# Optimization experiments

Hardware: AMD Instinct MI355X
Metric: run time of the kernel (lower is better)

Reference implementation:

```python
import jax, jax.numpy as jnp
import numpy as np

PAD = 16      # ReplicationPad2d(16)
KW = 33       # per-block kernel is 33x33
PATCH = 36    # 36x36 input patch per 4x4 output block
BLK = 4       # output block size


def setup_inputs() -> dict:
    key = jax.random.key(0)
    k1, k2 = jax.random.split(key)
    inputImg = jax.random.normal(k1, (1, 3, 512, 512), dtype=jnp.float32)
    Kernels = jax.random.uniform(k2, (1, KW * KW, 512 // BLK, 512 // BLK), dtype=jnp.float32)
    return {"inputImg": inputImg, "Kernels": Kernels}


def reference(inputImg, Kernels):
    B, C, H, W = inputImg.shape
    HB, WB = H // BLK, W // BLK
    # replication pad == edge pad
    padded = jnp.pad(inputImg, ((0, 0), (0, 0), (PAD, PAD), (PAD, PAD)), mode="edge")
    # gather overlapping 36x36 patches, one per 4x4 block (stride 4)
    idx_h = BLK * jnp.arange(HB)[:, None] + jnp.arange(PATCH)[None, :]  # [HB,36]
    idx_w = BLK * jnp.arange(WB)[:, None] + jnp.arange(PATCH)[None, :]  # [WB,36]
    tmp = padded[:, :, idx_h, :]            # [B,C,HB,36,Wp]
    patches = tmp[:, :, :, :, idx_w]        # [B,C,HB,36,WB,36]
    # per-block 33x33 kernel: Kernels[0, u*33+v, h, w] -> K[u,v,h,w]
    K = Kernels[0].reshape(KW, KW, HB, WB)
    # valid conv: out offset (oi,oj) in the 4x4 block
    rows = []
    for oi in range(BLK):
        cols = []
        for oj in range(BLK):
            win = patches[:, :, :, oi:oi + KW, :, oj:oj + KW]  # [B,C,HB,33,WB,33]
            cols.append(jnp.einsum("bchuwv,uvhw->bchw", win, K))
        rows.append(jnp.stack(cols, axis=-1))   # [B,C,HB,WB,4]
    out = jnp.stack(rows, axis=-2)              # [B,C,HB,WB,4,4]
    out = out.transpose(0, 1, 2, 4, 3, 5).reshape(B, C, H, W)
    return out
```

## Files before the change

### kernel.cpp

```cpp
#include <hip/hip_runtime.h>

#define HH 512
#define WW 512
#define PD 544
#define PADN (3 * PD * PD)
#define OUTN (3 * HH * WW)
#define NB 128
#define KSTR 16384

__global__ __launch_bounds__(256) void pad_kernel(const float* __restrict__ img,
                                                  unsigned short* __restrict__ gpad,
                                                  float* __restrict__ out) {
    int idx = blockIdx.x * 256 + threadIdx.x;
    if (idx < OUTN) out[idx] = 0.0f;
    if (idx >= PADN) return;
    int c  = idx / (PD * PD);
    int r  = idx - c * (PD * PD);
    int py = r / PD;
    int px = r - py * PD;
    int iy = min(max(py - 16, 0), HH - 1);
    int ix = min(max(px - 16, 0), WW - 1);
    union { float f; unsigned u; } v;
    v.f = img[(c * HH + iy) * WW + ix];
    unsigned u = v.u + 0x7FFFu + ((v.u >> 16) & 1u);
    gpad[idx] = (unsigned short)(u >> 16);
}

__device__ __forceinline__ void async4(const float* g, float* l) {
    __builtin_amdgcn_global_load_lds((const __attribute__((address_space(1))) void*)g,
                                     (__attribute__((address_space(3))) void*)l, 4, 0, 0);
}
__device__ __forceinline__ void async16u(const unsigned short* g, unsigned short* l) {
    __builtin_amdgcn_global_load_lds((const __attribute__((address_space(1))) void*)g,
                                     (__attribute__((address_space(3))) void*)l, 16, 0, 0);
}

__device__ __forceinline__ float bflo(unsigned d) {
    union { unsigned u; float f; } x; x.u = d << 16; return x.f;
}
__device__ __forceinline__ float bfhi(unsigned d) {
    union { unsigned u; float f; } x; x.u = d & 0xFFFF0000u; return x.f;
}

__global__ __launch_bounds__(64) void reblur_kernel(const unsigned short* __restrict__ gpad,
                                                    const float* __restrict__ Kern,
                                                    float* __restrict__ out) {
    __shared__ float s_w[4][33][64];
    __shared__ unsigned short s_img[2][3][296];

    const int lane = threadIdx.x;
    const int s    = blockIdx.x >> 8;
    const int bb   = blockIdx.x & 255;
    const int h    = bb >> 1;
    const int wt   = bb & 1;
    const int p0   = 12 * s;
    const int p1   = p0 + 12;
    const int kofs = h * NB + wt * 64 + lane;

    for (int u = max(0, p0 - 3); u <= p0; ++u)
        for (int v = 0; v < 33; ++v)
            async4(Kern + ((u * 33 + v) * KSTR + kofs), &s_w[u & 3][v][0]);
    if (lane < 36)
        for (int c = 0; c < 3; ++c)
            async16u(gpad + ((size_t)(c * PD + 4 * h + p0) * PD + 256 * wt) + 8 * lane,
                     &s_img[p0 & 1][c][0]);

    float acc[3][4][4];
#pragma unroll
    for (int c = 0; c < 3; ++c)
#pragma unroll
        for (int dy = 0; dy < 4; ++dy)
#pragma unroll
            for (int oj = 0; oj < 4; ++oj) acc[c][dy][oj] = 0.0f;

#pragma unroll 1
    for (int pp = p0; pp < p1; ++pp) {
        asm volatile("s_waitcnt vmcnt(0)" ::: "memory");

        float wreg[33];
        const int u3 = pp - 3;
        if (u3 >= 0) {
#pragma unroll
            for (int v = 0; v < 33; ++v) wreg[v] = s_w[u3 & 3][v][lane];
        }
        asm volatile("s_waitcnt lgkmcnt(0)" ::: "memory");

        if (pp + 1 < p1) {
            const int un = pp + 1;
            if (un <= 32)
                for (int v = 0; v < 33; ++v)
                    async4(Kern + ((un * 33 + v) * KSTR + kofs), &s_w[un & 3][v][0]);
            if (lane < 36)
                for (int c = 0; c < 3; ++c)
                    async16u(gpad + ((size_t)(c * PD + 4 * h + un) * PD + 256 * wt) + 8 * lane,
                             &s_img[un & 1][c][0]);
        }

        float wf[3][36];
        const int slot = pp & 1;
#pragma unroll
        for (int c = 0; c < 3; ++c) {
#pragma unroll
            for (int j = 0; j < 9; ++j) {
                const uint2 d = *(const uint2*)&s_img[slot][c][4 * lane + 4 * j];
                wf[c][4 * j + 0] = bflo(d.x);
                wf[c][4 * j + 1] = bfhi(d.x);
                wf[c][4 * j + 2] = bflo(d.y);
                wf[c][4 * j + 3] = bfhi(d.y);
            }
        }

#pragma unroll
        for (int dy = 0; dy < 3; ++dy) {
            const int u = pp - dy;
            if (u >= 0 && u <= 32) {
                const float* wp = &s_w[u & 3][0][lane];
#pragma unroll
                for (int v = 0; v < 33; ++v) {
                    const float w = wp[v * 64];
#pragma unroll
                    for (int c = 0; c < 3; ++c)
#pragma unroll
                        for (int oj = 0; oj < 4; ++oj)
                            acc[c][dy][oj] = fmaf(wf[c][v + oj], w, acc[c][dy][oj]);
                }
            }
        }
        if (u3 >= 0) {
#pragma unroll
            for (int v = 0; v < 33; ++v) {
#pragma unroll
                for (int c = 0; c < 3; ++c)
#pragma unroll
                    for (int oj = 0; oj < 4; ++oj)
                        acc[c][3][oj] = fmaf(wf[c][v + oj], wreg[v], acc[c][3][oj]);
            }
        }
    }

#pragma unroll
    for (int c = 0; c < 3; ++c)
#pragma unroll
        for (int dy = 0; dy < 4; ++dy) {
            float* op = out + (size_t)(c * HH + 4 * h + dy) * WW + 4 * (wt * 64 + lane);
#pragma unroll
            for (int oj = 0; oj < 4; ++oj) atomicAdd(op + oj, acc[c][dy][oj]);
        }
}

__global__ __launch_bounds__(256) void reblur_naive(const float* __restrict__ img,
                                                    const float* __restrict__ Kern,
                                                    float* __restrict__ out) {
    const int lane = threadIdx.x & 63;
    const int dy   = threadIdx.x >> 6;
    const int c    = blockIdx.x >> 8;
    const int bb   = blockIdx.x & 255;
    const int h    = bb >> 1;
    const int wt   = bb & 1;
    const int wb   = wt * 64 + lane;
    const int y    = 4 * h + dy;

    float acc[4] = {0.f, 0.f, 0.f, 0.f};
    const float* kb = Kern + h * NB + wb;
#pragma unroll 1
    for (int u = 0; u < 33; ++u) {
        const int iy = min(max(y + u - 16, 0), HH - 1);
        float row[36];
#pragma unroll
        for (int e = 0; e < 36; ++e) {
            const int ix = min(max(4 * wb + e - 16, 0), WW - 1);
            row[e]       = img[(c * HH + iy) * WW + ix];
        }
#pragma unroll
        for (int v = 0; v < 33; ++v) {
            const float w = kb[(u * 33 + v) * KSTR];
#pragma unroll
            for (int oj = 0; oj < 4; ++oj)
                acc[oj] = fmaf(row[v + oj], w, acc[oj]);
        }
    }
    float4 o;
    o.x = acc[0]; o.y = acc[1]; o.z = acc[2]; o.w = acc[3];
    *reinterpret_cast<float4*>(out + (size_t)(c * HH + y) * WW + 4 * wb) = o;
}

extern "C" void kernel_launch(void* const* d_in, const int* in_sizes, int n_in,
                              void* d_out, int out_size, void* d_ws, size_t ws_size,
                              hipStream_t stream) {
    const float* img  = (const float*)d_in[0];
    const float* Kern = (const float*)d_in[1];
    float* out        = (float*)d_out;

    if (ws_size >= (size_t)PADN * sizeof(unsigned short)) {
        unsigned short* gpad = (unsigned short*)d_ws;
        pad_kernel<<<(PADN + 255) / 256, 256, 0, stream>>>(img, gpad, out);
        reblur_kernel<<<768, 64, 0, stream>>>(gpad, Kern, out);
    } else {
        reblur_naive<<<768, 256, 0, stream>>>(img, Kern, out);
    }
}
```

Baseline: 160.1 us.

## Split output rows across two waves per block and partition kernel rows into four chunks

The reblur kernel now uses 128-thread blocks in which each wave owns two of the four output rows of a block. Kernel-row loading is split between the waves: one streams weights into LDS while the other streams image rows into a 4-deep ring. The u-range is split into four chunks (9/8/8/8) over 1024 blocks, replacing three 12-row chunks over 768 blocks. Weights are double-buffered in registers so each loaded row serves two output rows. This cuts per-thread accumulator and register pressure and raises parallelism, at the cost of a block-wide barrier every step and more atomic adds to the output.

```diff
diff --git a/kernel.cpp b/kernel.cpp
--- a/kernel.cpp
+++ b/kernel.cpp
@@ -34,118 +34,124 @@
     __builtin_amdgcn_global_load_lds((const __attribute__((address_space(1))) void*)g,
                                      (__attribute__((address_space(3))) void*)l, 16, 0, 0);
 }
-
-__device__ __forceinline__ float bflo(unsigned d) {
-    union { unsigned u; float f; } x; x.u = d << 16; return x.f;
-}
-__device__ __forceinline__ float bfhi(unsigned d) {
-    union { unsigned u; float f; } x; x.u = d & 0xFFFF0000u; return x.f;
-}
-
-__global__ __launch_bounds__(64) void reblur_kernel(const unsigned short* __restrict__ gpad,
-                                                    const float* __restrict__ Kern,
-                                                    float* __restrict__ out) {
-    __shared__ float s_w[4][33][64];
-    __shared__ unsigned short s_img[2][3][296];
-
-    const int lane = threadIdx.x;
-    const int s    = blockIdx.x >> 8;
-    const int bb   = blockIdx.x & 255;
-    const int h    = bb >> 1;
-    const int wt   = bb & 1;
-    const int p0   = 12 * s;
-    const int p1   = p0 + 12;
-    const int kofs = h * NB + wt * 64 + lane;
-
-    for (int u = max(0, p0 - 3); u <= p0; ++u)
+__device__ __forceinline__ float bflo(unsigned d) { union { unsigned u; float f; } x; x.u = d << 16;         return x.f; }
+__device__ __forceinline__ float bfhi(unsigned d) { union { unsigned u; float f; } x; x.u = d & 0xFFFF0000u; return x.f; }
+
+__global__ __launch_bounds__(128, 3) void reblur_kernel(const unsigned short* __restrict__ gpad,
+                                                        const float* __restrict__ Kern,
+                                                        float* __restrict__ out) {
+    __shared__ float s_w[2][33][64];
+    __shared__ unsigned short s_img[4][3][296];
+
+    const int lane   = threadIdx.x & 63;
+    const int pairId = threadIdx.x >> 6;
+    const int d0     = 2 * pairId;
+    const int uq     = blockIdx.x >> 8;
+    const int bb     = blockIdx.x & 255;
+    const int h      = bb >> 1;
+    const int wt     = bb & 1;
+    const int ua     = (uq == 0) ? 0 : (1 + 8 * uq);
+    const int n      = (uq == 0) ? 9 : 8;
+    const int kofs   = h * NB + wt * 64 + lane;
+    const int rbase  = 4 * h + ua;
+
+    if (pairId == 0) {
+#pragma unroll
         for (int v = 0; v < 33; ++v)
-            async4(Kern + ((u * 33 + v) * KSTR + kofs), &s_w[u & 3][v][0]);
-    if (lane < 36)
-        for (int c = 0; c < 3; ++c)
-            async16u(gpad + ((size_t)(c * PD + 4 * h + p0) * PD + 256 * wt) + 8 * lane,
-                     &s_img[p0 & 1][c][0]);
-
-    float acc[3][4][4];
+            async4(Kern + ((ua * 33 + v) * KSTR + kofs), &s_w[0][v][0]);
+    } else if (lane < 36) {
+#pragma unroll
+        for (int rr = 0; rr < 3; ++rr)
+#pragma unroll
+            for (int c = 0; c < 3; ++c)
+                async16u(gpad + ((size_t)(c * PD + rbase + rr) * PD + 256 * wt) + 8 * lane,
+                         &s_img[(rbase + rr) & 3][c][0]);
+    }
+
+    float wA[33], wB[33];
+    float accE[3][4], accO[3][4];
 #pragma unroll
     for (int c = 0; c < 3; ++c)
 #pragma unroll
-        for (int dy = 0; dy < 4; ++dy)
-#pragma unroll
-            for (int oj = 0; oj < 4; ++oj) acc[c][dy][oj] = 0.0f;
+        for (int oj = 0; oj < 4; ++oj) { accE[c][oj] = 0.f; accO[c][oj] = 0.f; }
+
+    auto body = [&](int t, int par, float (&wnew)[33], float (&wold)[33]) {
+        asm volatile("s_waitcnt vmcnt(0)" ::: "memory");
+        __builtin_amdgcn_s_barrier();
+        asm volatile("" ::: "memory");
+
+        const bool doE = (t < n);
+        const bool doO = (t > 0);
+
+        if (doE) {
+            if (pairId == 0) {
+                const int un = ua + t + 1;
+                if (t + 1 < n) {
+#pragma unroll
+                    for (int v = 0; v < 33; ++v)
+                        async4(Kern + ((un * 33 + v) * KSTR + kofs), &s_w[par ^ 1][v][0]);
+                }
+            } else if (lane < 36) {
+                const int r = rbase + t + 3;
+#pragma unroll
+                for (int c = 0; c < 3; ++c)
+                    async16u(gpad + ((size_t)(c * PD + r) * PD + 256 * wt) + 8 * lane,
+                             &s_img[r & 3][c][0]);
+            }
+        }
+
+        if (doE) {
+#pragma unroll
+            for (int v = 0; v < 33; ++v) wnew[v] = s_w[par][v][lane];
+        }
+
+        const int slot = (rbase + d0 + t) & 3;
+#pragma unroll
+        for (int c = 0; c < 3; ++c) {
+            float wf[36];
+            const unsigned short* sp = &s_img[slot][c][4 * lane];
+#pragma unroll
+            for (int j = 0; j < 9; ++j) {
+                const uint2 dd = *(const uint2*)(sp + 4 * j);
+                wf[4 * j + 0] = bflo(dd.x);
+                wf[4 * j + 1] = bfhi(dd.x);
+                wf[4 * j + 2] = bflo(dd.y);
+                wf[4 * j + 3] = bfhi(dd.y);
+            }
+            if (doE) {
+#pragma unroll
+                for (int v = 0; v < 33; ++v)
+#pragma unroll
+                    for (int oj = 0; oj < 4; ++oj)
+                        accE[c][oj] = fmaf(wf[v + oj], wnew[v], accE[c][oj]);
+            }
+            if (doO) {
+#pragma unroll
+                for (int v = 0; v < 33; ++v)
+#pragma unroll
+                    for (int oj = 0; oj < 4; ++oj)
+                        accO[c][oj] = fmaf(wf[v + oj], wold[v], accO[c][oj]);
+            }
+        }
+    };
 
 #pragma unroll 1
-    for (int pp = p0; pp < p1; ++pp) {
-        asm volatile("s_waitcnt vmcnt(0)" ::: "memory");
-
-        float wreg[33];
-        const int u3 = pp - 3;
-        if (u3 >= 0) {
-#pragma unroll
-            for (int v = 0; v < 33; ++v) wreg[v] = s_w[u3 & 3][v][lane];
-        }
-        asm volatile("s_waitcnt lgkmcnt(0)" ::: "memory");
-
-        if (pp + 1 < p1) {
-            const int un = pp + 1;
-            if (un <= 32)
-                for (int v = 0; v < 33; ++v)
-                    async4(Kern + ((un * 33 + v) * KSTR + kofs), &s_w[un & 3][v][0]);
-            if (lane < 36)
-                for (int c = 0; c < 3; ++c)
-                    async16u(gpad + ((size_t)(c * PD + 4 * h + un) * PD + 256 * wt) + 8 * lane,
-                             &s_img[un & 1][c][0]);
-        }
-
-        float wf[3][36];
-        const int slot = pp & 1;
-#pragma unroll
-        for (int c = 0; c < 3; ++c) {
-#pragma unroll
-            for (int j = 0; j < 9; ++j) {
-                const uint2 d = *(const uint2*)&s_img[slot][c][4 * lane + 4 * j];
-                wf[c][4 * j + 0] = bflo(d.x);
-                wf[c][4 * j + 1] = bfhi(d.x);
-                wf[c][4 * j + 2] = bflo(d.y);
-                wf[c][4 * j + 3] = bfhi(d.y);
-            }
-        }
-
-#pragma unroll
-        for (int dy = 0; dy < 3; ++dy) {
-            const int u = pp - dy;
-            if (u >= 0 && u <= 32) {
-                const float* wp = &s_w[u & 3][0][lane];
-#pragma unroll
-                for (int v = 0; v < 33; ++v) {
-                    const float w = wp[v * 64];
-#pragma unroll
-                    for (int c = 0; c < 3; ++c)
-#pragma unroll
-                        for (int oj = 0; oj < 4; ++oj)
-                            acc[c][dy][oj] = fmaf(wf[c][v + oj], w, acc[c][dy][oj]);
-                }
-            }
-        }
-        if (u3 >= 0) {
-#pragma unroll
-            for (int v = 0; v < 33; ++v) {
-#pragma unroll
-                for (int c = 0; c < 3; ++c)
-#pragma unroll
-                    for (int oj = 0; oj < 4; ++oj)
-                        acc[c][3][oj] = fmaf(wf[c][v + oj], wreg[v], acc[c][3][oj]);
-            }
-        }
-    }
-
-#pragma unroll
-    for (int c = 0; c < 3; ++c)
-#pragma unroll
-        for (int dy = 0; dy < 4; ++dy) {
-            float* op = out + (size_t)(c * HH + 4 * h + dy) * WW + 4 * (wt * 64 + lane);
-#pragma unroll
-            for (int oj = 0; oj < 4; ++oj) atomicAdd(op + oj, acc[c][dy][oj]);
-        }
+    for (int t2 = 0; t2 <= n; t2 += 2) {
+        body(t2, 0, wA, wB);
+        if (t2 + 1 <= n) body(t2 + 1, 1, wB, wA);
+    }
+
+    const int xb = 4 * (wt * 64 + lane);
+#pragma unroll
+    for (int c = 0; c < 3; ++c) {
+        float* opE = out + (size_t)(c * HH + 4 * h + d0) * WW + xb;
+        float* opO = opE + WW;
+#pragma unroll
+        for (int oj = 0; oj < 4; ++oj) {
+            atomicAdd(opE + oj, accE[c][oj]);
+            atomicAdd(opO + oj, accO[c][oj]);
+        }
+    }
 }
 
 __global__ __launch_bounds__(256) void reblur_naive(const float* __restrict__ img,
@@ -194,7 +200,7 @@
     if (ws_size >= (size_t)PADN * sizeof(unsigned short)) {
         unsigned short* gpad = (unsigned short*)d_ws;
         pad_kernel<<<(PADN + 255) / 256, 256, 0, stream>>>(img, gpad, out);
-        reblur_kernel<<<768, 64, 0, stream>>>(gpad, Kern, out);
+        reblur_kernel<<<1024, 128, 0, stream>>>(gpad, Kern, out);
     } else {
         reblur_naive<<<768, 256, 0, stream>>>(img, Kern, out);
     }
```

After: 301.5 us. 1.88x slower.

## Restructure reblur into 4-wave blocks splitting kernel rows, weights in registers

Applied to the files above, without the earlier changes.

The reblur kernel now uses 256-thread blocks where each wave handles one output row offset dy, and the 33 kernel rows are split into two halves (17/16) across blocks instead of three 12-row passes. Kernel weights are loaded straight into double-buffered registers instead of staged through LDS, and image rows go into an 8-slot LDS ring shared by the four waves with block barriers. The aim is to cut LDS weight traffic and redundant weight reads, raise occupancy and halve the atomic partial sums. The cost is block-level synchronisation each step and direct global weight loads whose latency must hide behind compute.

```diff
diff --git a/kernel.cpp b/kernel.cpp
--- a/kernel.cpp
+++ b/kernel.cpp
@@ -26,126 +26,104 @@
     gpad[idx] = (unsigned short)(u >> 16);
 }
 
-__device__ __forceinline__ void async4(const float* g, float* l) {
-    __builtin_amdgcn_global_load_lds((const __attribute__((address_space(1))) void*)g,
-                                     (__attribute__((address_space(3))) void*)l, 4, 0, 0);
-}
 __device__ __forceinline__ void async16u(const unsigned short* g, unsigned short* l) {
     __builtin_amdgcn_global_load_lds((const __attribute__((address_space(1))) void*)g,
                                      (__attribute__((address_space(3))) void*)l, 16, 0, 0);
 }
+__device__ __forceinline__ float bflo(unsigned d) { union { unsigned u; float f; } x; x.u = d << 16;         return x.f; }
+__device__ __forceinline__ float bfhi(unsigned d) { union { unsigned u; float f; } x; x.u = d & 0xFFFF0000u; return x.f; }
 
-__device__ __forceinline__ float bflo(unsigned d) {
-    union { unsigned u; float f; } x; x.u = d << 16; return x.f;
-}
-__device__ __forceinline__ float bfhi(unsigned d) {
-    union { unsigned u; float f; } x; x.u = d & 0xFFFF0000u; return x.f;
-}
+__global__ __launch_bounds__(256, 2) void reblur_kernel(const unsigned short* __restrict__ gpad,
+                                                        const float* __restrict__ Kern,
+                                                        float* __restrict__ out) {
+    __shared__ unsigned short s_img[8][3][288];
 
-__global__ __launch_bounds__(64) void reblur_kernel(const unsigned short* __restrict__ gpad,
-                                                    const float* __restrict__ Kern,
-                                                    float* __restrict__ out) {
-    __shared__ float s_w[4][33][64];
-    __shared__ unsigned short s_img[2][3][296];
-
-    const int lane = threadIdx.x;
-    const int s    = blockIdx.x >> 8;
+    const int lane = threadIdx.x & 63;
+    const int dy   = threadIdx.x >> 6;
+    const int uq   = blockIdx.x >> 8;
     const int bb   = blockIdx.x & 255;
     const int h    = bb >> 1;
     const int wt   = bb & 1;
-    const int p0   = 12 * s;
-    const int p1   = p0 + 12;
+    const int ua   = 17 * uq;
+    const int n    = 17 - uq;
     const int kofs = h * NB + wt * 64 + lane;
 
-    for (int u = max(0, p0 - 3); u <= p0; ++u)
-        for (int v = 0; v < 33; ++v)
-            async4(Kern + ((u * 33 + v) * KSTR + kofs), &s_w[u & 3][v][0]);
-    if (lane < 36)
+    if (lane < 36) {
+        const int r = 4 * h + ua + dy;
+#pragma unroll
         for (int c = 0; c < 3; ++c)
-            async16u(gpad + ((size_t)(c * PD + 4 * h + p0) * PD + 256 * wt) + 8 * lane,
-                     &s_img[p0 & 1][c][0]);
+            async16u(gpad + ((size_t)(c * PD + r) * PD + 256 * wt) + 8 * lane,
+                     &s_img[r & 7][c][0]);
+    }
+    float wA[33], wB[33];
+#pragma unroll
+    for (int v = 0; v < 33; ++v)
+        wA[v] = Kern[(size_t)(ua * 33 + v) * KSTR + kofs];
 
-    float acc[3][4][4];
+    float acc[3][4];
 #pragma unroll
     for (int c = 0; c < 3; ++c)
 #pragma unroll
-        for (int dy = 0; dy < 4; ++dy)
-#pragma unroll
-            for (int oj = 0; oj < 4; ++oj) acc[c][dy][oj] = 0.0f;
+        for (int oj = 0; oj < 4; ++oj) acc[c][oj] = 0.0f;
 
-#pragma unroll 1
-    for (int pp = p0; pp < p1; ++pp) {
-        asm volatile("s_waitcnt vmcnt(0)" ::: "memory");
-
-        float wreg[33];
-        const int u3 = pp - 3;
-        if (u3 >= 0) {
-#pragma unroll
-            for (int v = 0; v < 33; ++v) wreg[v] = s_w[u3 & 3][v][lane];
-        }
-        asm volatile("s_waitcnt lgkmcnt(0)" ::: "memory");
-
-        if (pp + 1 < p1) {
-            const int un = pp + 1;
-            if (un <= 32)
-                for (int v = 0; v < 33; ++v)
-                    async4(Kern + ((un * 33 + v) * KSTR + kofs), &s_w[un & 3][v][0]);
-            if (lane < 36)
-                for (int c = 0; c < 3; ++c)
-                    async16u(gpad + ((size_t)(c * PD + 4 * h + un) * PD + 256 * wt) + 8 * lane,
-                             &s_img[un & 1][c][0]);
-        }
-
-        float wf[3][36];
-        const int slot = pp & 1;
-#pragma unroll
-        for (int c = 0; c < 3; ++c) {
-#pragma unroll
-            for (int j = 0; j < 9; ++j) {
-                const uint2 d = *(const uint2*)&s_img[slot][c][4 * lane + 4 * j];
-                wf[c][4 * j + 0] = bflo(d.x);
-                wf[c][4 * j + 1] = bfhi(d.x);
-                wf[c][4 * j + 2] = bflo(d.y);
-                wf[c][4 * j + 3] = bfhi(d.y);
-            }
-        }
-
-#pragma unroll
-        for (int dy = 0; dy < 3; ++dy) {
-            const int u = pp - dy;
-            if (u >= 0 && u <= 32) {
-                const float* wp = &s_w[u & 3][0][lane];
-#pragma unroll
-                for (int v = 0; v < 33; ++v) {
-                    const float w = wp[v * 64];
-#pragma unroll
-                    for (int c = 0; c < 3; ++c)
-#pragma unroll
-                        for (int oj = 0; oj < 4; ++oj)
-                            acc[c][dy][oj] = fmaf(wf[c][v + oj], w, acc[c][dy][oj]);
-                }
-            }
-        }
-        if (u3 >= 0) {
-#pragma unroll
-            for (int v = 0; v < 33; ++v) {
-#pragma unroll
-                for (int c = 0; c < 3; ++c)
-#pragma unroll
-                    for (int oj = 0; oj < 4; ++oj)
-                        acc[c][3][oj] = fmaf(wf[c][v + oj], wreg[v], acc[c][3][oj]);
-            }
-        }
+#define R6_ITER(WCUR, WNXT, TT)                                                  \
+    {                                                                            \
+        const int tt = (TT);                                                     \
+        asm volatile("s_waitcnt vmcnt(0)" ::: "memory");                         \
+        __builtin_amdgcn_s_barrier();                                            \
+        if (tt + 1 < n) {                                                        \
+            const int un = ua + tt + 1;                                          \
+            _Pragma("unroll")                                                    \
+            for (int v = 0; v < 33; ++v)                                         \
+                WNXT[v] = Kern[(size_t)(un * 33 + v) * KSTR + kofs];             \
+            if (dy == (tt & 3) && lane < 36) {                                   \
+                const int r = 4 * h + ua + tt + 4;                               \
+                _Pragma("unroll")                                                \
+                for (int c = 0; c < 3; ++c)                                      \
+                    async16u(gpad + ((size_t)(c * PD + r) * PD + 256 * wt) + 8 * lane, \
+                             &s_img[r & 7][c][0]);                               \
+            }                                                                    \
+        }                                                                        \
+        const int slot = (4 * h + ua + tt + dy) & 7;                             \
+        _Pragma("unroll")                                                        \
+        for (int c = 0; c < 3; ++c) {                                            \
+            float wf[36];                                                        \
+            const unsigned short* sp = &s_img[slot][c][4 * lane];                \
+            _Pragma("unroll")                                                    \
+            for (int j = 0; j < 9; ++j) {                                        \
+                const uint2 dd = *(const uint2*)(sp + 4 * j);                    \
+                wf[4 * j + 0] = bflo(dd.x);                                      \
+                wf[4 * j + 1] = bfhi(dd.x);                                      \
+                wf[4 * j + 2] = bflo(dd.y);                                      \
+                wf[4 * j + 3] = bfhi(dd.y);                                      \
+            }                                                                    \
+            _Pragma("unroll")                                                    \
+            for (int v = 0; v < 33; ++v) {                                       \
+                _Pragma("unroll")                                                \
+                for (int oj = 0; oj < 4; ++oj)                                   \
+                    acc[c][oj] = fmaf(wf[v + oj], WCUR[v], acc[c][oj]);          \
+            }                                                                    \
+        }                                                                        \
     }
 
+    int t = 0;
+#pragma unroll 1
+    for (; t + 1 < n; t += 2) {
+        R6_ITER(wA, wB, t);
+        R6_ITER(wB, wA, t + 1);
+    }
+    if (t < n) {
+        R6_ITER(wA, wB, t);
+    }
+#undef R6_ITER
+
+    const int xb = 4 * (wt * 64 + lane);
 #pragma unroll
-    for (int c = 0; c < 3; ++c)
+    for (int c = 0; c < 3; ++c) {
+        float* op = out + (size_t)(c * HH + 4 * h + dy) * WW + xb;
 #pragma unroll
-        for (int dy = 0; dy < 4; ++dy) {
-            float* op = out + (size_t)(c * HH + 4 * h + dy) * WW + 4 * (wt * 64 + lane);
-#pragma unroll
-            for (int oj = 0; oj < 4; ++oj) atomicAdd(op + oj, acc[c][dy][oj]);
-        }
+        for (int oj = 0; oj < 4; ++oj) atomicAdd(op + oj, acc[c][oj]);
+    }
 }
 
 __global__ __launch_bounds__(256) void reblur_naive(const float* __restrict__ img,
@@ -194,7 +172,7 @@
     if (ws_size >= (size_t)PADN * sizeof(unsigned short)) {
         unsigned short* gpad = (unsigned short*)d_ws;
         pad_kernel<<<(PADN + 255) / 256, 256, 0, stream>>>(img, gpad, out);
-        reblur_kernel<<<768, 64, 0, stream>>>(gpad, Kern, out);
+        reblur_kernel<<<512, 256, 0, stream>>>(gpad, Kern, out);
     } else {
         reblur_naive<<<768, 256, 0, stream>>>(img, Kern, out);
     }
```

Result: faster. 145.7 us (-9.0%).
